# Kernel optimization log

Hardware: AMD Instinct MI355X
Metric: run time of the kernel (lower is better)

Reference implementation:

```python
import jax, jax.numpy as jnp
import numpy as np

# CrossAttention (DFFNet): 1x1 convs produce q,k from depth and v from rgb;
# full dense attention over hw spatial tokens: softmax(q^T k) then v @ mask^T.

def setup_inputs() -> dict:
    key = jax.random.key(0)
    ks = jax.random.split(key, 8)
    B, C, H, W = 4, 256, 64, 64
    Cqk = C // 8  # ratio=8 -> 32
    s = 0.02
    return {
        "rgb":   jax.random.normal(ks[0], (B, C, H, W), jnp.float32),
        "depth": jax.random.normal(ks[1], (B, C, H, W), jnp.float32),
        "Wq": jax.random.normal(ks[2], (Cqk, C), jnp.float32) * s,
        "bq": jax.random.normal(ks[3], (Cqk,), jnp.float32) * s,
        "Wk": jax.random.normal(ks[4], (Cqk, C), jnp.float32) * s,
        "bk": jax.random.normal(ks[5], (Cqk,), jnp.float32) * s,
        "Wv": jax.random.normal(ks[6], (C, C), jnp.float32) * s,
        "bv": jax.random.normal(ks[7], (C,), jnp.float32) * s,
    }


def reference(rgb, depth, Wq, bq, Wk, bk, Wv, bv):
    B, C, H, W = rgb.shape
    hw = H * W
    d = depth.reshape(B, C, hw)   # [B, C, hw]
    r = rgb.reshape(B, C, hw)     # [B, C, hw]
    # 1x1 convs == channel-mixing linear maps
    q = jnp.einsum('oc,bcn->bon', Wq, d) + bq[None, :, None]  # [B, Cqk, hw]
    k = jnp.einsum('oc,bcn->bon', Wk, d) + bk[None, :, None]  # [B, Cqk, hw]
    v = jnp.einsum('oc,bcn->bon', Wv, r) + bv[None, :, None]  # [B, C, hw]
    # scores: q^T k -> [B, hw, hw], softmax over last dim
    scores = jnp.einsum('bcn,bcm->bnm', q, k)
    mask = jax.nn.softmax(scores, axis=-1)
    # feat = v @ mask^T  -> [B, C, hw]
    feat = jnp.einsum('bcm,bnm->bcn', v, mask)
    return feat.reshape(B, C, H, W)
```

## Files before the change

kernel.cpp:

```cpp
#include <hip/hip_runtime.h>
#include <stdint.h>

#define L2E 1.44269504088896340736f

typedef _Float16 half8 __attribute__((ext_vector_type(8)));
typedef float floatx4 __attribute__((ext_vector_type(4)));

static __device__ __forceinline__ unsigned short f32_to_f16u(float f) {
  union { _Float16 h; unsigned short s; } cv; cv.h = (_Float16)f; return cv.s;
}

__global__ __launch_bounds__(256) void proj_kernel(
    const float* __restrict__ rgb,
    const float* __restrict__ depth,
    const float* __restrict__ Wq, const float* __restrict__ bq,
    const float* __restrict__ Wk, const float* __restrict__ bk,
    const float* __restrict__ Wv, const float* __restrict__ bv,
    unsigned short* __restrict__ qT,
    unsigned short* __restrict__ kT,
    unsigned short* __restrict__ v)
{
  __shared__ __align__(16) unsigned short sW[64 * 256];

  const int n0 = blockIdx.x * 64;
  const int b  = blockIdx.y;
  const int z  = blockIdx.z;
  const int t  = threadIdx.x;
  const int w  = t >> 6;
  const int lane = t & 63;
  const int l15 = lane & 15;
  const int q4  = lane >> 4;

  const float* X = (z == 0) ? depth : rgb;
  const float* xb = X + (size_t)b * 256 * 4096;
  const int n_row = n0 + 16 * w + l15;
  const int colbase = (z == 0) ? 0 : (z - 1) * 64;

#pragma unroll
  for (int it = 0; it < 8; it++) {
    int L = it * 256 + t;
    int og = L >> 5;
    int phys = L & 31;
    int ci = phys ^ (og & 7);
    const float* wr;
    if (z == 0) wr = (og < 32) ? (Wq + (size_t)og * 256) : (Wk + (size_t)(og - 32) * 256);
    else        wr = Wv + (size_t)(colbase + og) * 256;
    float4 w0 = *(const float4*)(wr + ci * 8);
    float4 w1 = *(const float4*)(wr + ci * 8 + 4);
    half8 h;
    h[0] = (_Float16)w0.x; h[1] = (_Float16)w0.y; h[2] = (_Float16)w0.z; h[3] = (_Float16)w0.w;
    h[4] = (_Float16)w1.x; h[5] = (_Float16)w1.y; h[6] = (_Float16)w1.z; h[7] = (_Float16)w1.w;
    *(half8*)&sW[(size_t)L * 8] = h;
  }

  float bias[4];
#pragma unroll
  for (int ct = 0; ct < 4; ct++) {
    int og = ct * 16 + l15;
    if (z == 0) bias[ct] = (og < 32) ? bq[og] : bk[og - 32];
    else        bias[ct] = bv[colbase + og];
  }
  __syncthreads();

  floatx4 acc[4];
#pragma unroll
  for (int i = 0; i < 4; i++) acc[i] = (floatx4){0.f, 0.f, 0.f, 0.f};

#pragma unroll
  for (int ks = 0; ks < 8; ks++) {
    const int c0 = ks * 32;
    half8 a;
#pragma unroll
    for (int j = 0; j < 8; j++) {
      int c = c0 + q4 * 8 + j;
      a[j] = (_Float16)xb[(size_t)c * 4096 + n_row];
    }
    const int ci = ks * 4 + q4;
#pragma unroll
    for (int ct = 0; ct < 4; ct++) {
      int og = ct * 16 + l15;
      half8 bf = *(const half8*)&sW[og * 256 + ((ci ^ (og & 7)) * 8)];
      acc[ct] = __builtin_amdgcn_mfma_f32_16x16x32_f16(a, bf, acc[ct], 0, 0, 0);
    }
  }

  __syncthreads();

  if (z == 0) {
#pragma unroll
    for (int ct = 0; ct < 4; ct++) {
      int og = ct * 16 + l15;
#pragma unroll
      for (int r = 0; r < 4; r++) {
        int n = n0 + 16 * w + q4 * 4 + r;
        unsigned short hv = f32_to_f16u(acc[ct][r] + bias[ct]);
        if (og < 32) qT[((size_t)b * 4096 + n) * 32 + og] = hv;
        else         kT[((size_t)b * 4096 + n) * 32 + (og - 32)] = hv;
      }
    }
  } else {
    unsigned short* tile = sW;
#pragma unroll
    for (int ct = 0; ct < 4; ct++) {
#pragma unroll
      for (int r = 0; r < 4; r++) {
        int co_l = ct * 16 + l15;
        int nl = 16 * w + q4 * 4 + r;
        tile[co_l * 72 + nl] = f32_to_f16u(acc[ct][r] + bias[ct]);
      }
    }
    __syncthreads();
#pragma unroll
    for (int it = 0; it < 2; it++) {
      int co_l = it * 32 + (t >> 3);
      int ch = t & 7;
      int4 val = *(const int4*)&tile[co_l * 72 + ch * 8];
      *(int4*)&v[((size_t)b * 256 + colbase + co_l) * 4096 + n0 + ch * 8] = val;
    }
  }
}

__global__ __launch_bounds__(256, 4) void attn_kernel(
    const unsigned short* __restrict__ qT,
    const unsigned short* __restrict__ kT,
    const unsigned short* __restrict__ v,
    unsigned short* __restrict__ Op,
    float* __restrict__ lW)
{
  __shared__ __align__(16) unsigned char smem[36864];
  unsigned short* sV = (unsigned short*)smem;
  unsigned short* sK = (unsigned short*)(smem + 16384);
  unsigned short* sP = (unsigned short*)(smem + 18432);

  const int n0 = blockIdx.x * 64;
  const int b  = blockIdx.y;
  const int chunk = blockIdx.z;
  const int t  = threadIdx.x;
  const int w  = t >> 6;
  const int lane = t & 63;
  const int l15 = lane & 15;
  const int q4  = lane >> 4;

  const unsigned short* qrow = qT + ((size_t)b * 4096 + n0 + 16 * w + l15) * 32 + q4 * 8;
  half8 aq = *(const half8*)qrow;

  const unsigned short* vB = v  + (size_t)b * 256 * 4096;
  const unsigned short* kB = kT + (size_t)b * 4096 * 32;
  unsigned short* sPw = sP + w * 640;

  float lsum[4] = {0.f, 0.f, 0.f, 0.f};
  floatx4 acc[16];
#pragma unroll
  for (int ct = 0; ct < 16; ct++) acc[ct] = (floatx4){0.f, 0.f, 0.f, 0.f};
  const floatx4 zf = (floatx4){0.f, 0.f, 0.f, 0.f};

  const int mbase = chunk * 1024;
  for (int mi = 0; mi < 1024; mi += 32) {
    const int m0 = mbase + mi;
    __syncthreads();
#pragma unroll
    for (int j = 0; j < 4; j++) {
      int lin = j * 256 + t;
      int c = lin >> 2;
      int p = lin & 3;
      int lc = p ^ ((c >> 1) & 3);
      uint4 val = *(const uint4*)&vB[(size_t)c * 4096 + m0 + lc * 8];
      *(uint4*)&sV[lin * 8] = val;
    }
    if (t < 128) {
      int m = t >> 2, p = t & 3, lc = p ^ ((m >> 1) & 3);
      uint4 val = *(const uint4*)&kB[(size_t)(m0 + m) * 32 + lc * 8];
      *(uint4*)&sK[t * 8] = val;
    }
    __syncthreads();

    half8 bk0 = *(const half8*)&sK[l15 * 32 + ((q4 ^ ((l15 >> 1) & 3)) * 8)];
    half8 bk1 = *(const half8*)&sK[(16 + l15) * 32 + ((q4 ^ (((16 + l15) >> 1) & 3)) * 8)];
    floatx4 s0 = __builtin_amdgcn_mfma_f32_16x16x32_f16(aq, bk0, zf, 0, 0, 0);
    floatx4 s1 = __builtin_amdgcn_mfma_f32_16x16x32_f16(aq, bk1, zf, 0, 0, 0);

    float p0[4], p1[4];
#pragma unroll
    for (int r = 0; r < 4; r++) {
      p0[r] = exp2f(s0[r] * L2E);
      p1[r] = exp2f(s1[r] * L2E);
      lsum[r] += p0[r] + p1[r];
    }
#pragma unroll
    for (int r = 0; r < 4; r++) {
      int row = q4 * 4 + r;
      sPw[row * 40 + l15]      = f32_to_f16u(p0[r]);
      sPw[row * 40 + 16 + l15] = f32_to_f16u(p1[r]);
    }
    asm volatile("s_waitcnt lgkmcnt(0)" ::: "memory");
    half8 ap = *(const half8*)&sPw[l15 * 40 + q4 * 8];
#pragma unroll
    for (int ct = 0; ct < 16; ct++) {
      int co = ct * 16 + l15;
      half8 bv8 = *(const half8*)&sV[co * 32 + ((q4 ^ ((co >> 1) & 3)) * 8)];
      acc[ct] = __builtin_amdgcn_mfma_f32_16x16x32_f16(ap, bv8, acc[ct], 0, 0, 0);
    }
  }

#pragma unroll
  for (int off = 1; off < 16; off <<= 1) {
#pragma unroll
    for (int r = 0; r < 4; r++) lsum[r] += __shfl_xor(lsum[r], off);
  }
  if (l15 == 0) {
#pragma unroll
    for (int r = 0; r < 4; r++)
      lW[((size_t)chunk * 4 + b) * 4096 + n0 + 16 * w + q4 * 4 + r] = lsum[r];
  }

  unsigned short* sO = (unsigned short*)smem;
#pragma unroll
  for (int pass = 0; pass < 2; pass++) {
    __syncthreads();
#pragma unroll
    for (int cl = 0; cl < 8; cl++) {
      int ct = pass * 8 + cl;
      int co_l = cl * 16 + l15;
#pragma unroll
      for (int r = 0; r < 4; r++) {
        int nl = 16 * w + q4 * 4 + r;
        sO[co_l * 72 + nl] = f32_to_f16u(acc[ct][r]);
      }
    }
    __syncthreads();
#pragma unroll
    for (int s = 0; s < 4; s++) {
      int co_l = s * 32 + (t >> 3);
      int ch = t & 7;
      int4 val = *(const int4*)&sO[co_l * 72 + ch * 8];
      *(int4*)&Op[(((size_t)chunk * 4 + b) * 256 + pass * 128 + co_l) * 4096 + n0 + ch * 8] = val;
    }
  }
}

__global__ __launch_bounds__(256) void combine_kernel(
    const unsigned short* __restrict__ Op,
    const float* __restrict__ lW,
    float* __restrict__ out)
{
  const int t = threadIdx.x;
  const int b = blockIdx.y;
  const size_t n8 = (size_t)blockIdx.x * 2048 + (size_t)t * 8;
  const int co0 = blockIdx.z * 8;

  float sum[8] = {0.f, 0.f, 0.f, 0.f, 0.f, 0.f, 0.f, 0.f};
#pragma unroll
  for (int ch = 0; ch < 4; ch++) {
    const float* lp = lW + ((size_t)ch * 4 + b) * 4096 + n8;
    float4 a0 = *(const float4*)lp;
    float4 a1 = *(const float4*)(lp + 4);
    sum[0] += a0.x; sum[1] += a0.y; sum[2] += a0.z; sum[3] += a0.w;
    sum[4] += a1.x; sum[5] += a1.y; sum[6] += a1.z; sum[7] += a1.w;
  }
  float rl[8];
#pragma unroll
  for (int i = 0; i < 8; i++) rl[i] = 1.0f / sum[i];

#pragma unroll
  for (int cc = 0; cc < 8; cc++) {
    int co = co0 + cc;
    float o[8] = {0.f, 0.f, 0.f, 0.f, 0.f, 0.f, 0.f, 0.f};
#pragma unroll
    for (int ch = 0; ch < 4; ch++) {
      half8 hv = *(const half8*)&Op[(((size_t)ch * 4 + b) * 256 + co) * 4096 + n8];
#pragma unroll
      for (int i = 0; i < 8; i++) o[i] += (float)hv[i];
    }
    float* op = out + ((size_t)b * 256 + co) * 4096 + n8;
    float4 r0, r1;
    r0.x = o[0] * rl[0]; r0.y = o[1] * rl[1]; r0.z = o[2] * rl[2]; r0.w = o[3] * rl[3];
    r1.x = o[4] * rl[4]; r1.y = o[5] * rl[5]; r1.z = o[6] * rl[6]; r1.w = o[7] * rl[7];
    *(float4*)op = r0;
    *(float4*)(op + 4) = r1;
  }
}

extern "C" void kernel_launch(void* const* d_in, const int* in_sizes, int n_in,
                              void* d_out, int out_size, void* d_ws, size_t ws_size,
                              hipStream_t stream) {
  const float* rgb   = (const float*)d_in[0];
  const float* depth = (const float*)d_in[1];
  const float* Wq    = (const float*)d_in[2];
  const float* bq    = (const float*)d_in[3];
  const float* Wk    = (const float*)d_in[4];
  const float* bk    = (const float*)d_in[5];
  const float* Wv    = (const float*)d_in[6];
  const float* bv    = (const float*)d_in[7];
  float* out = (float*)d_out;

  unsigned short* qT = (unsigned short*)d_ws;
  unsigned short* kT = qT + (size_t)4 * 4096 * 32;
  unsigned short* vW = kT + (size_t)4 * 4096 * 32;
  unsigned short* Op = vW + (size_t)4 * 256 * 4096;
  float* lW = (float*)(Op + (size_t)4 * 4 * 256 * 4096);

  dim3 pg(64, 4, 5);
  proj_kernel<<<pg, 256, 0, stream>>>(rgb, depth, Wq, bq, Wk, bk, Wv, bv, qT, kT, vW);
  dim3 ag(64, 4, 4);
  attn_kernel<<<ag, 256, 0, stream>>>(qT, kT, vW, Op, lW);
  dim3 cg(2, 4, 32);
  combine_kernel<<<cg, 256, 0, stream>>>(Op, lW, out);
}
```

Measured before the change: 171.3 us.

## Double-buffer V tiles with async global-to-LDS loads and register-prefetch K

Replaces the synchronous V staging (global load into registers, then LDS store) with global_load_lds direct-to-LDS copies into a double buffer, prefetching the next tile while the current one is consumed. K fragments are now loaded straight from global into registers one iteration ahead, no longer staged through shared memory. The aim is to hide global load latency behind the MFMA work and cut register traffic. In exchange it relies on hand-placed vmcnt/lgkmcnt waits and raw s_barrier calls, and shared memory grows slightly.

```diff
diff --git a/kernel.cpp b/kernel.cpp
--- a/kernel.cpp
+++ b/kernel.cpp
@@ -8,6 +8,13 @@
 
 static __device__ __forceinline__ unsigned short f32_to_f16u(float f) {
   union { _Float16 h; unsigned short s; } cv; cv.h = (_Float16)f; return cv.s;
+}
+
+typedef __attribute__((address_space(3))) unsigned int as3_uint;
+typedef __attribute__((address_space(1))) const unsigned int as1_cuint;
+
+static __device__ __forceinline__ void async16(const void* g, void* l) {
+  __builtin_amdgcn_global_load_lds((as1_cuint*)g, (as3_uint*)l, 16, 0, 0);
 }
 
 __global__ __launch_bounds__(256) void proj_kernel(
@@ -120,6 +127,20 @@
   }
 }
 
+static __device__ __forceinline__ void stage_v(
+    const unsigned short* __restrict__ vB, unsigned char* sbase,
+    int m0, int t, int w)
+{
+#pragma unroll
+  for (int j = 0; j < 4; j++) {
+    int lin = j * 256 + t;
+    int c = lin >> 2;
+    int p = lin & 3;
+    int lc = p ^ ((c >> 1) & 3);
+    async16(&vB[(size_t)c * 4096 + m0 + lc * 8], sbase + j * 4096 + w * 1024);
+  }
+}
+
 __global__ __launch_bounds__(256, 4) void attn_kernel(
     const unsigned short* __restrict__ qT,
     const unsigned short* __restrict__ kT,
@@ -127,10 +148,8 @@
     unsigned short* __restrict__ Op,
     float* __restrict__ lW)
 {
-  __shared__ __align__(16) unsigned char smem[36864];
-  unsigned short* sV = (unsigned short*)smem;
-  unsigned short* sK = (unsigned short*)(smem + 16384);
-  unsigned short* sP = (unsigned short*)(smem + 18432);
+  __shared__ __align__(16) unsigned char smem[37888];
+  unsigned short* sP = (unsigned short*)(smem + 32768);
 
   const int n0 = blockIdx.x * 64;
   const int b  = blockIdx.y;
@@ -141,11 +160,10 @@
   const int l15 = lane & 15;
   const int q4  = lane >> 4;
 
-  const unsigned short* qrow = qT + ((size_t)b * 4096 + n0 + 16 * w + l15) * 32 + q4 * 8;
-  half8 aq = *(const half8*)qrow;
-
-  const unsigned short* vB = v  + (size_t)b * 256 * 4096;
-  const unsigned short* kB = kT + (size_t)b * 4096 * 32;
+  half8 aq = *(const half8*)(qT + ((size_t)b * 4096 + n0 + 16 * w + l15) * 32 + q4 * 8);
+
+  const unsigned short* vB = v + (size_t)b * 256 * 4096;
+  const unsigned short* kL = kT + (size_t)b * 4096 * 32 + (size_t)l15 * 32 + q4 * 8;
   unsigned short* sPw = sP + w * 640;
 
   float lsum[4] = {0.f, 0.f, 0.f, 0.f};
@@ -155,29 +173,26 @@
   const floatx4 zf = (floatx4){0.f, 0.f, 0.f, 0.f};
 
   const int mbase = chunk * 1024;
-  for (int mi = 0; mi < 1024; mi += 32) {
-    const int m0 = mbase + mi;
-    __syncthreads();
-#pragma unroll
-    for (int j = 0; j < 4; j++) {
-      int lin = j * 256 + t;
-      int c = lin >> 2;
-      int p = lin & 3;
-      int lc = p ^ ((c >> 1) & 3);
-      uint4 val = *(const uint4*)&vB[(size_t)c * 4096 + m0 + lc * 8];
-      *(uint4*)&sV[lin * 8] = val;
-    }
-    if (t < 128) {
-      int m = t >> 2, p = t & 3, lc = p ^ ((m >> 1) & 3);
-      uint4 val = *(const uint4*)&kB[(size_t)(m0 + m) * 32 + lc * 8];
-      *(uint4*)&sK[t * 8] = val;
-    }
-    __syncthreads();
-
-    half8 bk0 = *(const half8*)&sK[l15 * 32 + ((q4 ^ ((l15 >> 1) & 3)) * 8)];
-    half8 bk1 = *(const half8*)&sK[(16 + l15) * 32 + ((q4 ^ (((16 + l15) >> 1) & 3)) * 8)];
-    floatx4 s0 = __builtin_amdgcn_mfma_f32_16x16x32_f16(aq, bk0, zf, 0, 0, 0);
-    floatx4 s1 = __builtin_amdgcn_mfma_f32_16x16x32_f16(aq, bk1, zf, 0, 0, 0);
+
+  stage_v(vB, smem, mbase, t, w);
+  half8 kc0 = *(const half8*)(kL + (size_t)mbase * 32);
+  half8 kc1 = *(const half8*)(kL + (size_t)(mbase + 16) * 32);
+
+  int bufoff = 0;
+  for (int it = 0; it < 32; ++it) {
+    const int m0 = mbase + it * 32;
+    half8 kn0 = kc0, kn1 = kc1;
+    if (it < 31) {
+      stage_v(vB, smem + (bufoff ^ 16384), m0 + 32, t, w);
+      kn0 = *(const half8*)(kL + (size_t)(m0 + 32) * 32);
+      kn1 = *(const half8*)(kL + (size_t)(m0 + 48) * 32);
+      asm volatile("s_waitcnt vmcnt(6)" ::: "memory");
+    } else {
+      asm volatile("s_waitcnt vmcnt(0)" ::: "memory");
+    }
+
+    floatx4 s0 = __builtin_amdgcn_mfma_f32_16x16x32_f16(aq, kc0, zf, 0, 0, 0);
+    floatx4 s1 = __builtin_amdgcn_mfma_f32_16x16x32_f16(aq, kc1, zf, 0, 0, 0);
 
     float p0[4], p1[4];
 #pragma unroll
@@ -194,12 +209,22 @@
     }
     asm volatile("s_waitcnt lgkmcnt(0)" ::: "memory");
     half8 ap = *(const half8*)&sPw[l15 * 40 + q4 * 8];
+
+    __builtin_amdgcn_s_barrier();
+    asm volatile("s_waitcnt lgkmcnt(0)" ::: "memory");
+
+    const unsigned short* sVb = (const unsigned short*)(smem + bufoff);
 #pragma unroll
     for (int ct = 0; ct < 16; ct++) {
       int co = ct * 16 + l15;
-      half8 bv8 = *(const half8*)&sV[co * 32 + ((q4 ^ ((co >> 1) & 3)) * 8)];
+      half8 bv8 = *(const half8*)&sVb[co * 32 + ((q4 ^ ((co >> 1) & 3)) * 8)];
       acc[ct] = __builtin_amdgcn_mfma_f32_16x16x32_f16(ap, bv8, acc[ct], 0, 0, 0);
     }
+    asm volatile("s_waitcnt lgkmcnt(0)" ::: "memory");
+    __builtin_amdgcn_s_barrier();
+
+    kc0 = kn0; kc1 = kn1;
+    bufoff ^= 16384;
   }
 
 #pragma unroll
```

After: 168.1 us. About the same (-1.9%).
